# Kernel tuning notes

Measured on AMD Instinct MI355X. Metric: run time of the kernel, lower is better.

The kernel has to match this reference:

```python
import jax, jax.numpy as jnp
import numpy as np
from jax import lax

EPS = 1e-5

def bn(x, g, b):
    # training-mode BatchNorm2d over (N, H, W)
    m = jnp.mean(x, axis=(0, 2, 3), keepdims=True)
    v = jnp.var(x, axis=(0, 2, 3), keepdims=True)
    return (x - m) * lax.rsqrt(v + EPS) * g[None, :, None, None] + b[None, :, None, None]

def conv1x1(x, W):
    # x: [b,c,h,w], W: [o,c]
    return jnp.einsum('bchw,oc->bohw', x, W)

def conv3x3(x, W):
    # W: [o,i,3,3]
    return lax.conv_general_dilated(x, W, (1, 1), 'SAME',
                                    dimension_numbers=('NCHW', 'OIHW', 'NCHW'))

def lga(x, Wqkv, Wproj, g, b):
    # LinearGlobalAttention: O(N) global attention
    bsz, c, h, w = x.shape
    qkv = conv1x1(x, Wqkv)                       # [b, 3c, h, w]
    q, k, v = jnp.split(qkv, 3, axis=1)
    q = q.reshape(bsz, c, h * w)                 # [b, c, N]
    k = jax.nn.softmax(k.reshape(bsz, c, h * w), axis=-1)
    v = v.reshape(bsz, c, h * w)
    ctx = jnp.einsum('bcn,bdn->bcd', k, v)       # [b, c, c]
    out = jnp.einsum('bcd,bcn->bdn', ctx, q)     # context^T @ q -> [b, c, N]
    out = out.reshape(bsz, c, h, w)
    return jax.nn.relu(bn(conv1x1(out, Wproj), g, b))


def setup_inputs() -> dict:
    key = jax.random.key(0)
    ks = jax.random.split(key, 12)
    B, Cin, Cout, H, W = 16, 128, 256, 64, 64
    wd = Cout // 4  # branch width = 64
    sc = 0.05
    inp = {
        'x': jax.random.normal(ks[0], (B, Cin, H, W), jnp.float32),
        'W_sc': jax.random.normal(ks[1], (Cout, Cin), jnp.float32) * sc,
        'g_sc': jnp.ones((Cout,), jnp.float32),
        'b_sc': jnp.zeros((Cout,), jnp.float32),
        'W1': jax.random.normal(ks[2], (Cout, Cin), jnp.float32) * sc,
        'g1': jnp.ones((Cout,), jnp.float32),
        'b1': jnp.zeros((Cout,), jnp.float32),
        'Wb0': jax.random.normal(ks[3], (wd, wd), jnp.float32) * sc,
        'gb0': jnp.ones((wd,), jnp.float32),
        'bb0': jnp.zeros((wd,), jnp.float32),
        'Wb1': jax.random.normal(ks[4], (wd, wd, 3, 3), jnp.float32) * sc,
        'gb1': jnp.ones((wd,), jnp.float32),
        'bb1': jnp.zeros((wd,), jnp.float32),
        'Wqkv2': jax.random.normal(ks[5], (3 * wd, wd), jnp.float32) * sc,
        'Wproj2': jax.random.normal(ks[6], (wd, wd), jnp.float32) * sc,
        'ga2': jnp.ones((wd,), jnp.float32),
        'ba2': jnp.zeros((wd,), jnp.float32),
        'Wqkv3': jax.random.normal(ks[7], (3 * wd, wd), jnp.float32) * sc,
        'Wproj3': jax.random.normal(ks[8], (wd, wd), jnp.float32) * sc,
        'ga3': jnp.ones((wd,), jnp.float32),
        'ba3': jnp.zeros((wd,), jnp.float32),
        'W2': jax.random.normal(ks[9], (Cout, Cout), jnp.float32) * sc,
        'g2': jnp.ones((Cout,), jnp.float32),
        'b2': jnp.zeros((Cout,), jnp.float32),
    }
    return inp


def reference(x, W_sc, g_sc, b_sc, W1, g1, b1,
              Wb0, gb0, bb0, Wb1, gb1, bb1,
              Wqkv2, Wproj2, ga2, ba2,
              Wqkv3, Wproj3, ga3, ba3,
              W2, g2, b2):
    residual = bn(conv1x1(x, W_sc), g_sc, b_sc)
    h = jax.nn.relu(bn(conv1x1(x, W1), g1, b1))      # [b, 256, H, W]
    s0, s1, s2, s3 = jnp.split(h, 4, axis=1)          # width = 64 each
    o0 = jax.nn.relu(bn(conv1x1(s0, Wb0), gb0, bb0))  # k=1 branch
    o1 = jax.nn.relu(bn(conv3x3(s1, Wb1), gb1, bb1))  # k=3 branch
    o2 = lga(s2, Wqkv2, Wproj2, ga2, ba2)             # k=5 -> attention
    o3 = lga(s3, Wqkv3, Wproj3, ga3, ba3)             # k=7 -> attention
    out = jnp.concatenate([o0, o1, o2, o3], axis=1)
    out = bn(conv1x1(out, W2), g2, b2) + residual
    return jax.nn.relu(out)
```

## Files before the change

kernel.cpp:

```cpp
#include <hip/hip_runtime.h>
#include <hip/hip_bf16.h>

using bf16 = __hip_bfloat16;
typedef __bf16 bf16v8 __attribute__((ext_vector_type(8)));
typedef float f32x4 __attribute__((ext_vector_type(4)));

#define HW 4096
#define ROWS 65536
#define BRSTRIDE 4194304

#define AS1 const __attribute__((address_space(1))) void*
#define AS3 __attribute__((address_space(3))) void*

__global__ void r4_cvt_w(const float* __restrict__ Wsc, const float* __restrict__ W1,
                         const float* __restrict__ Wb0,
                         const float* __restrict__ Wqkv2, const float* __restrict__ Wqkv3,
                         const float* __restrict__ W2, const float* __restrict__ Wb1,
                         bf16* __restrict__ wbase, bf16* __restrict__ wp,
                         float* __restrict__ stats) {
    int i = blockIdx.x * 256 + threadIdx.x;
    if (i < 2048) stats[i] = 0.f;
    if (i < 159744) {
        const float* s; int off;
        if      (i < 32768)  { s = Wsc;   off = i; }
        else if (i < 65536)  { s = W1;    off = i - 32768; }
        else if (i < 69632)  { s = Wb0;   off = i - 65536; }
        else if (i < 81920)  { s = Wqkv2; off = i - 69632; }
        else if (i < 94208)  { s = Wqkv3; off = i - 81920; }
        else                 { s = W2;    off = i - 94208; }
        wbase[i] = __float2bfloat16(s[off]);
    } else {
        int k = i - 159744;
        int tap = k / 4096, rem = k % 4096;
        int o = rem >> 6, c = rem & 63;
        wp[k] = __float2bfloat16(Wb1[(size_t)(o * 64 + c) * 9 + tap]);
    }
}

__global__ void r4_cvt_x(const float* __restrict__ x, bf16* __restrict__ xT) {
    __shared__ bf16 tile[64 * 65];
    int b = blockIdx.z, c0 = blockIdx.y * 64, n0 = blockIdx.x * 64;
    int t = threadIdx.x;
#pragma unroll
    for (int i = 0; i < 4; i++) {
        int idx = i * 256 + t;
        int cc = idx >> 4, n4 = (idx & 15) * 4;
        float4 v = *(const float4*)&x[((size_t)(b * 128 + c0 + cc)) * HW + n0 + n4];
        tile[(n4 + 0) * 65 + cc] = __float2bfloat16(v.x);
        tile[(n4 + 1) * 65 + cc] = __float2bfloat16(v.y);
        tile[(n4 + 2) * 65 + cc] = __float2bfloat16(v.z);
        tile[(n4 + 3) * 65 + cc] = __float2bfloat16(v.w);
    }
    __syncthreads();
#pragma unroll
    for (int i = 0; i < 2; i++) {
        int u = i * 256 + t;
        int nn = u >> 3, p = u & 7;
        bf16v8 v;
#pragma unroll
        for (int j = 0; j < 8; j++) v[j] = (__bf16)tile[nn * 65 + p * 8 + j];
        *(bf16v8*)&xT[((size_t)(b * HW + n0 + nn)) * 128 + c0 + p * 8] = v;
    }
}

template <int KK>
__global__ __launch_bounds__(256) void ga_gemm(
        const bf16* __restrict__ A, int a_stride,
        const bf16* __restrict__ W, int w_stride,
        bf16* __restrict__ out0, bf16* __restrict__ out1, int split,
        int out_stride,
        float* __restrict__ stat0, float* __restrict__ stat1,
        int scol0, int scol1,
        const float* __restrict__ tsums,
        const float* __restrict__ tg0, const float* __restrict__ tb0,
        const float* __restrict__ tg1, const float* __restrict__ tb1,
        const float* __restrict__ tg2, const float* __restrict__ tb2,
        const float* __restrict__ tg3, const float* __restrict__ tb3) {
    __shared__ bf16 shmem[128 * 136];
    __shared__ float sredS[256], sredQ[256];
    __shared__ float scS[256], shS[256];
    bf16* As = shmem;
    bf16* Ws = shmem + 8192;

    int t = threadIdx.x;
    int wave = t >> 6, lane = t & 63;
    int lo = lane & 15, quad = lane >> 4;
    int wr = wave >> 1, wc = wave & 1;
    int b = blockIdx.z;
    long grow = (long)b * HW + blockIdx.x * 128;
    int o0 = blockIdx.y * 128;
    const bf16* Wb = W + (long)o0 * w_stride;

    if (tsums) {
        int qi = t >> 6, ci = t & 63;
        const float* gp = qi == 0 ? tg0 : qi == 1 ? tg1 : qi == 2 ? tg2 : tg3;
        const float* bp = qi == 0 ? tb0 : qi == 1 ? tb1 : qi == 2 ? tb2 : tb3;
        float mean = tsums[t] * (1.f / 65536.f);
        float var  = tsums[256 + t] * (1.f / 65536.f) - mean * mean;
        float s = gp[ci] * rsqrtf(var + 1e-5f);
        scS[t] = s; shS[t] = bp[ci] - mean * s;
    }

    f32x4 acc[4][4];
#pragma unroll
    for (int m = 0; m < 4; m++)
#pragma unroll
        for (int n = 0; n < 4; n++) acc[m][n] = (f32x4){0.f, 0.f, 0.f, 0.f};

#pragma unroll
    for (int ph = 0; ph < KK / 64; ph++) {
        int k0 = ph * 64;
#pragma unroll
        for (int j = 0; j < 4; j++) {
            int i = j * 4 + wave;
            int ci = i * 64 + lane;
            int R = ci >> 3, cc = ci & 7;
            int sw = ((cc ^ (R & 7)) << 3);
            __builtin_amdgcn_global_load_lds(
                (AS1)(A + (grow + R) * (long)a_stride + k0 + sw),
                (AS3)(As + i * 512), 16, 0, 0);
            __builtin_amdgcn_global_load_lds(
                (AS1)(Wb + (long)R * w_stride + k0 + sw),
                (AS3)(Ws + i * 512), 16, 0, 0);
        }
        asm volatile("s_waitcnt vmcnt(0)" ::: "memory");
        __syncthreads();
        if (tsums) {
#pragma unroll
            for (int i = 0; i < 4; i++) {
                int ci = i * 256 + t;
                int R = ci >> 3, p = ci & 7;
                int chb = k0 + ((p ^ (R & 7)) << 3);
                bf16v8 v = *(const bf16v8*)&As[R * 64 + p * 8];
#pragma unroll
                for (int j = 0; j < 8; j++) {
                    float f = (float)v[j] * scS[chb + j] + shS[chb + j];
                    v[j] = (__bf16)fmaxf(f, 0.f);
                }
                *(bf16v8*)&As[R * 64 + p * 8] = v;
            }
            __syncthreads();
        }
#pragma unroll
        for (int ks = 0; ks < 64; ks += 32) {
            int kk = (ks >> 3) + quad;
            bf16v8 av[4], wv[4];
#pragma unroll
            for (int m = 0; m < 4; m++) {
                int R = wr * 64 + m * 16 + lo;
                av[m] = *(const bf16v8*)&As[R * 64 + ((kk ^ (R & 7)) << 3)];
            }
#pragma unroll
            for (int n = 0; n < 4; n++) {
                int R = wc * 64 + n * 16 + lo;
                wv[n] = *(const bf16v8*)&Ws[R * 64 + ((kk ^ (R & 7)) << 3)];
            }
#pragma unroll
            for (int m = 0; m < 4; m++)
#pragma unroll
                for (int n = 0; n < 4; n++)
                    acc[m][n] = __builtin_amdgcn_mfma_f32_16x16x32_bf16(av[m], wv[n], acc[m][n], 0, 0, 0);
        }
        __syncthreads();
    }

    bf16* Ot = shmem;
#pragma unroll
    for (int m = 0; m < 4; m++)
#pragma unroll
        for (int n = 0; n < 4; n++)
#pragma unroll
            for (int r = 0; r < 4; r++)
                Ot[(wr * 64 + m * 16 + quad * 4 + r) * 136 + wc * 64 + n * 16 + lo] =
                    __float2bfloat16(acc[m][n][r]);
    __syncthreads();
    bool low = o0 < split;
    bf16* op = low ? out0 : out1;
    int oc0 = low ? o0 : o0 - split;
#pragma unroll
    for (int i = 0; i < 8; i++) {
        int u = i * 256 + t;
        int lr = u >> 4, cg = u & 15;
        *(bf16v8*)&op[(grow + lr) * (long)out_stride + oc0 + cg * 8] =
            *(const bf16v8*)&Ot[lr * 136 + cg * 8];
    }
    if (stat0) {
        int c = t & 127, half = t >> 7;
        float s = 0.f, q = 0.f;
#pragma unroll
        for (int r = 0; r < 64; r++) {
            float v = __bfloat162float(Ot[(half * 64 + r) * 136 + c]);
            s += v; q += v * v;
        }
        sredS[t] = s; sredQ[t] = q;
        __syncthreads();
        if (t < 128) {
            float ss = sredS[t] + sredS[t + 128];
            float qq = sredQ[t] + sredQ[t + 128];
            float* st = low ? stat0 : stat1;
            int ci = (low ? scol0 + o0 : scol1 + o0 - split) + c;
            atomicAdd(&st[ci], ss);
            atomicAdd(&st[256 + ci], qq);
        }
    }
}

__global__ __launch_bounds__(256) void gq_gemm(
        const bf16* __restrict__ y1,
        const bf16* __restrict__ wq2, const bf16* __restrict__ wq3,
        const bf16* __restrict__ wb0,
        bf16* __restrict__ qs, bf16* __restrict__ ks, bf16* __restrict__ vs,
        bf16* __restrict__ obuf, float* __restrict__ stats,
        const float* __restrict__ asums,
        const float* __restrict__ g1, const float* __restrict__ b1) {
    __shared__ bf16 shmem[128 * 64 + 64 * 64];
    __shared__ float scS[64], shS[64];
    bf16* As = shmem;
    bf16* Ws = shmem + 8192;
    float* sredS = (float*)(shmem + 9216);
    float* sredQ = sredS + 256;

    int t = threadIdx.x;
    int wave = t >> 6, lane = t & 63;
    int lo = lane & 15, quad = lane >> 4;
    int b = blockIdx.z, y = blockIdx.y;
    long grow = (long)b * HW + blockIdx.x * 128;

    const bf16* Ab; const bf16* Wb; bf16* outp; int ostride; float* st; int col0;
    if (y == 6) {
        Ab = y1; Wb = wb0; outp = obuf; ostride = 256; st = stats; col0 = 0;
    } else {
        int br = y / 3, sel = y - br * 3;
        col0 = 128 + br * 64;
        Ab = y1 + col0;
        Wb = (br ? wq3 : wq2) + sel * 4096;
        outp = (sel == 0 ? qs : sel == 1 ? ks : vs) + (long)br * BRSTRIDE;
        ostride = 64; st = nullptr;
    }
    if (t < 64) {
        int ch = col0 + t;
        float mean = asums[ch] * (1.f / 65536.f);
        float var  = asums[256 + ch] * (1.f / 65536.f) - mean * mean;
        float s = g1[ch] * rsqrtf(var + 1e-5f);
        scS[t] = s; shS[t] = b1[ch] - mean * s;
    }

    f32x4 acc[2][4];
#pragma unroll
    for (int m = 0; m < 2; m++)
#pragma unroll
        for (int n = 0; n < 4; n++) acc[m][n] = (f32x4){0.f, 0.f, 0.f, 0.f};

#pragma unroll
    for (int j = 0; j < 4; j++) {
        int i = j * 4 + wave;
        int ci = i * 64 + lane;
        int R = ci >> 3, cc = ci & 7;
        __builtin_amdgcn_global_load_lds(
            (AS1)(Ab + (grow + R) * 256L + ((cc ^ (R & 7)) << 3)),
            (AS3)(As + i * 512), 16, 0, 0);
    }
#pragma unroll
    for (int j = 0; j < 2; j++) {
        int ci = (j * 4 + wave) * 64 + lane;
        int R = ci >> 3, cc = ci & 7;
        __builtin_amdgcn_global_load_lds(
            (AS1)(Wb + R * 64 + ((cc ^ (R & 7)) << 3)),
            (AS3)(Ws + (j * 4 + wave) * 512), 16, 0, 0);
    }
    asm volatile("s_waitcnt vmcnt(0)" ::: "memory");
    __syncthreads();
#pragma unroll
    for (int i = 0; i < 4; i++) {
        int ci = i * 256 + t;
        int R = ci >> 3, p = ci & 7;
        int chb = (p ^ (R & 7)) << 3;
        bf16v8 v = *(const bf16v8*)&As[R * 64 + p * 8];
#pragma unroll
        for (int j = 0; j < 8; j++) {
            float f = (float)v[j] * scS[chb + j] + shS[chb + j];
            v[j] = (__bf16)fmaxf(f, 0.f);
        }
        *(bf16v8*)&As[R * 64 + p * 8] = v;
    }
    __syncthreads();

#pragma unroll
    for (int ks_ = 0; ks_ < 64; ks_ += 32) {
        int kk = (ks_ >> 3) + quad;
        bf16v8 av[2], wv[4];
#pragma unroll
        for (int m = 0; m < 2; m++) {
            int R = wave * 32 + m * 16 + lo;
            av[m] = *(const bf16v8*)&As[R * 64 + ((kk ^ (R & 7)) << 3)];
        }
#pragma unroll
        for (int n = 0; n < 4; n++) {
            int o = n * 16 + lo;
            wv[n] = *(const bf16v8*)&Ws[o * 64 + ((kk ^ (o & 7)) << 3)];
        }
#pragma unroll
        for (int m = 0; m < 2; m++)
#pragma unroll
            for (int n = 0; n < 4; n++)
                acc[m][n] = __builtin_amdgcn_mfma_f32_16x16x32_bf16(av[m], wv[n], acc[m][n], 0, 0, 0);
    }
    __syncthreads();

    bf16* Ot = shmem;
#pragma unroll
    for (int m = 0; m < 2; m++)
#pragma unroll
        for (int n = 0; n < 4; n++)
#pragma unroll
            for (int r = 0; r < 4; r++)
                Ot[(wave * 32 + m * 16 + quad * 4 + r) * 72 + n * 16 + lo] =
                    __float2bfloat16(acc[m][n][r]);
    __syncthreads();
#pragma unroll
    for (int i = 0; i < 4; i++) {
        int u = i * 256 + t;
        int lr = u >> 3, cg = u & 7;
        *(bf16v8*)&outp[(grow + lr) * (long)ostride + cg * 8] =
            *(const bf16v8*)&Ot[lr * 72 + cg * 8];
    }
    if (st) {
        int c = t & 63, qtr = t >> 6;
        float s = 0.f, q = 0.f;
#pragma unroll
        for (int r = 0; r < 32; r++) {
            float v = __bfloat162float(Ot[(qtr * 32 + r) * 72 + c]);
            s += v; q += v * v;
        }
        sredS[t] = s; sredQ[t] = q;
        __syncthreads();
        if (t < 64) {
            float ss = sredS[t] + sredS[t + 64] + sredS[t + 128] + sredS[t + 192];
            float qq = sredQ[t] + sredQ[t + 64] + sredQ[t + 128] + sredQ[t + 192];
            atomicAdd(&st[t], ss);
            atomicAdd(&st[256 + t], qq);
        }
    }
}

__global__ __launch_bounds__(256) void gp_gemm(
        const bf16* __restrict__ qs, const bf16* __restrict__ M,
        bf16* __restrict__ obuf, float* __restrict__ stats) {
    __shared__ bf16 shmem[128 * 64 + 64 * 64];
    bf16* As = shmem;
    bf16* Ws = shmem + 8192;
    float* sredS = (float*)(shmem + 9216);
    float* sredQ = sredS + 256;

    int t = threadIdx.x;
    int wave = t >> 6, lane = t & 63;
    int lo = lane & 15, quad = lane >> 4;
    int b = blockIdx.z, y = blockIdx.y;
    long grow = (long)b * HW + blockIdx.x * 128;
    const bf16* Ab = qs + (long)y * BRSTRIDE;
    const bf16* Wb = M + y * 65536 + (long)b * 4096;
    int oc0 = 128 + y * 64;

    f32x4 acc[2][4];
#pragma unroll
    for (int m = 0; m < 2; m++)
#pragma unroll
        for (int n = 0; n < 4; n++) acc[m][n] = (f32x4){0.f, 0.f, 0.f, 0.f};

#pragma unroll
    for (int j = 0; j < 4; j++) {
        int i = j * 4 + wave;
        int ci = i * 64 + lane;
        int R = ci >> 3, cc = ci & 7;
        __builtin_amdgcn_global_load_lds(
            (AS1)(Ab + (grow + R) * 64L + ((cc ^ (R & 7)) << 3)),
            (AS3)(As + i * 512), 16, 0, 0);
    }
#pragma unroll
    for (int j = 0; j < 2; j++) {
        int ci = (j * 4 + wave) * 64 + lane;
        int R = ci >> 3, cc = ci & 7;
        __builtin_amdgcn_global_load_lds(
            (AS1)(Wb + R * 64 + ((cc ^ (R & 7)) << 3)),
            (AS3)(Ws + (j * 4 + wave) * 512), 16, 0, 0);
    }
    asm volatile("s_waitcnt vmcnt(0)" ::: "memory");
    __syncthreads();

#pragma unroll
    for (int ks_ = 0; ks_ < 64; ks_ += 32) {
        int kk = (ks_ >> 3) + quad;
        bf16v8 av[2], wv[4];
#pragma unroll
        for (int m = 0; m < 2; m++) {
            int R = wave * 32 + m * 16 + lo;
            av[m] = *(const bf16v8*)&As[R * 64 + ((kk ^ (R & 7)) << 3)];
        }
#pragma unroll
        for (int n = 0; n < 4; n++) {
            int o = n * 16 + lo;
            wv[n] = *(const bf16v8*)&Ws[o * 64 + ((kk ^ (o & 7)) << 3)];
        }
#pragma unroll
        for (int m = 0; m < 2; m++)
#pragma unroll
            for (int n = 0; n < 4; n++)
                acc[m][n] = __builtin_amdgcn_mfma_f32_16x16x32_bf16(av[m], wv[n], acc[m][n], 0, 0, 0);
    }
    __syncthreads();

    bf16* Ot = shmem;
#pragma unroll
    for (int m = 0; m < 2; m++)
#pragma unroll
        for (int n = 0; n < 4; n++)
#pragma unroll
            for (int r = 0; r < 4; r++)
                Ot[(wave * 32 + m * 16 + quad * 4 + r) * 72 + n * 16 + lo] =
                    __float2bfloat16(acc[m][n][r]);
    __syncthreads();
#pragma unroll
    for (int i = 0; i < 4; i++) {
        int u = i * 256 + t;
        int lr = u >> 3, cg = u & 7;
        *(bf16v8*)&obuf[(grow + lr) * 256L + oc0 + cg * 8] =
            *(const bf16v8*)&Ot[lr * 72 + cg * 8];
    }
    {
        int c = t & 63, qtr = t >> 6;
        float s = 0.f, q = 0.f;
#pragma unroll
        for (int r = 0; r < 32; r++) {
            float v = __bfloat162float(Ot[(qtr * 32 + r) * 72 + c]);
            s += v; q += v * v;
        }
        sredS[t] = s; sredQ[t] = q;
        __syncthreads();
        if (t < 64) {
            float ss = sredS[t] + sredS[t + 64] + sredS[t + 128] + sredS[t + 192];
            float qq = sredQ[t] + sredQ[t + 64] + sredQ[t + 128] + sredQ[t + 192];
            atomicAdd(&stats[oc0 + t], ss);
            atomicAdd(&stats[256 + oc0 + t], qq);
        }
    }
}

__global__ __launch_bounds__(256) void r12_conv3(
        const bf16* __restrict__ hT, const bf16* __restrict__ wp,
        bf16* __restrict__ obuf, float* __restrict__ stat,
        const float* __restrict__ asums,
        const float* __restrict__ g1, const float* __restrict__ b1) {
    __shared__ bf16 As[6 * 66 * 64];
    __shared__ bf16 Wt[9 * 64 * 64];
    __shared__ float sredS[256], sredQ[256];
    __shared__ float scS[64], shS[64];

    int t = threadIdx.x;
    int wave = t >> 6, lane = t & 63;
    int lo = lane & 15, quad = lane >> 4;
    int b = blockIdx.y, y0 = blockIdx.x * 4;

    if (t < 64) {
        int ch = 64 + t;
        float mean = asums[ch] * (1.f / 65536.f);
        float var  = asums[256 + ch] * (1.f / 65536.f) - mean * mean;
        float s = g1[ch] * rsqrtf(var + 1e-5f);
        scS[t] = s; shS[t] = b1[ch] - mean * s;
    }

#pragma unroll
    for (int j = 0; j < 18; j++) {
        int i = j * 4 + wave;
        int ci = i * 64 + lane;
        int tap = ci >> 9, rem = ci & 511, o = rem >> 3, ck = rem & 7;
        __builtin_amdgcn_global_load_lds(
            (AS1)(wp + tap * 4096 + o * 64 + ((ck ^ (o & 7)) << 3)),
            (AS3)(Wt + i * 512), 16, 0, 0);
    }
#pragma unroll
    for (int j = 0; j < 12; j++) {
        int i = j * 4 + wave;
        int row = i >> 3, seg = i & 7;
        int yy = y0 - 1 + row;
        if (yy >= 0 && yy < 64) {
            int xg = seg * 8 + (lane >> 3), ck = lane & 7;
            __builtin_amdgcn_global_load_lds(
                (AS1)(hT + ((long)b * HW + yy * 64 + xg) * 256 + 64 + ((ck ^ (xg & 7)) << 3)),
                (AS3)(As + row * 4224 + 64 + seg * 512), 16, 0, 0);
        } else {
            *(bf16v8*)&As[row * 4224 + 64 + seg * 512 + lane * 8] = (bf16v8){0,0,0,0,0,0,0,0};
        }
    }
    if (t < 96) {
        int yr = t >> 4, side = (t >> 3) & 1, ck = t & 7;
        *(bf16v8*)&As[yr * 4224 + (side ? 65 : 0) * 64 + ck * 8] = (bf16v8){0,0,0,0,0,0,0,0};
    }
    asm volatile("s_waitcnt vmcnt(0)" ::: "memory");
    __syncthreads();
#pragma unroll
    for (int i = 0; i < 12; i++) {
        int ci = i * 256 + t;
        int row = ci >> 9, rem = ci & 511;
        int xg = rem >> 3, p = rem & 7;
        int yy = y0 - 1 + row;
        if (yy >= 0 && yy < 64) {
            int chb = (p ^ (xg & 7)) << 3;
            bf16v8 v = *(const bf16v8*)&As[row * 4224 + (xg + 1) * 64 + p * 8];
#pragma unroll
            for (int j = 0; j < 8; j++) {
                float f = (float)v[j] * scS[chb + j] + shS[chb + j];
                v[j] = (__bf16)fmaxf(f, 0.f);
            }
            *(bf16v8*)&As[row * 4224 + (xg + 1) * 64 + p * 8] = v;
        }
    }
    __syncthreads();

    f32x4 acc[4][4];
#pragma unroll
    for (int m = 0; m < 4; m++)
#pragma unroll
        for (int n = 0; n < 4; n++) acc[m][n] = (f32x4){0.f, 0.f, 0.f, 0.f};

#pragma unroll
    for (int tap = 0; tap < 9; tap++) {
        int dy = tap / 3 - 1, dx = tap % 3 - 1;
        int yr = wave + 1 + dy;
#pragma unroll
        for (int ks8 = 0; ks8 < 8; ks8 += 4) {
            int kk = ks8 + quad;
            bf16v8 wv[4];
#pragma unroll
            for (int ot = 0; ot < 4; ot++) {
                int o = ot * 16 + lo;
                wv[ot] = *(const bf16v8*)&Wt[tap * 4096 + o * 64 + ((kk ^ (o & 7)) << 3)];
            }
#pragma unroll
            for (int m = 0; m < 4; m++) {
                int xp = m * 16 + lo + dx;
                bf16v8 av = *(const bf16v8*)&As[yr * 4224 + (xp + 1) * 64 + ((kk ^ (xp & 7)) << 3)];
#pragma unroll
                for (int ot = 0; ot < 4; ot++)
                    acc[m][ot] = __builtin_amdgcn_mfma_f32_16x16x32_bf16(av, wv[ot], acc[m][ot], 0, 0, 0);
            }
        }
    }
    __syncthreads();

    bf16* Ot = As;
#pragma unroll
    for (int m = 0; m < 4; m++)
#pragma unroll
        for (int ot = 0; ot < 4; ot++)
#pragma unroll
            for (int r = 0; r < 4; r++)
                Ot[(wave * 64 + m * 16 + quad * 4 + r) * 72 + ot * 16 + lo] =
                    __float2bfloat16(acc[m][ot][r]);
    __syncthreads();

    long grow = (long)b * HW + y0 * 64;
#pragma unroll
    for (int i = 0; i < 8; i++) {
        int u = i * 256 + t;
        int lr = u >> 3, cg = u & 7;
        *(bf16v8*)&obuf[(grow + lr) * 256 + 64 + cg * 8] = *(const bf16v8*)&Ot[lr * 72 + cg * 8];
    }
    {
        int c = t & 63, qtr = t >> 6;
        float s = 0.f, q = 0.f;
#pragma unroll
        for (int r = 0; r < 64; r++) {
            float v = __bfloat162float(Ot[(qtr * 64 + r) * 72 + c]);
            s += v; q += v * v;
        }
        sredS[t] = s; sredQ[t] = q;
        __syncthreads();
        if (t < 64) {
            float ss = sredS[t] + sredS[t + 64] + sredS[t + 128] + sredS[t + 192];
            float qq = sredQ[t] + sredQ[t + 64] + sredQ[t + 128] + sredQ[t + 192];
            atomicAdd(&stat[64 + t], ss);
            atomicAdd(&stat[256 + 64 + t], qq);
        }
    }
}

__global__ __launch_bounds__(256) void r14_softctx(
        const bf16* __restrict__ ks_t, const bf16* __restrict__ vs_t,
        float* __restrict__ ctx_p, float* __restrict__ lpart) {
    __shared__ bf16 Ks[64 * 136];
    __shared__ bf16 Vs[64 * 136];
    float* red = (float*)Ks;
    int t = threadIdx.x;
    int wave = t >> 6, lane = t & 63;
    int lo = lane & 15, quad = lane >> 4;
    int b = blockIdx.y, bx = blockIdx.x, z = blockIdx.z;
    const bf16* kb = ks_t + (long)z * BRSTRIDE;
    const bf16* vb = vs_t + (long)z * BRSTRIDE;

    f32x4 acc[4];
#pragma unroll
    for (int ot = 0; ot < 4; ot++) acc[ot] = (f32x4){0.f, 0.f, 0.f, 0.f};
    float sm[8];
#pragma unroll
    for (int j = 0; j < 8; j++) sm[j] = 0.f;

    for (int it = 0; it < 2; it++) {
        long n0 = ((long)bx * 2 + it) * 128;
        __syncthreads();
#pragma unroll
        for (int sub = 0; sub < 4; sub++) {
            int r = sub * 32 + (t >> 3), cg = t & 7;
            long row = (long)b * HW + n0 + r;
            bf16v8 k8 = *(const bf16v8*)(kb + row * 64 + cg * 8);
            bf16v8 v8 = *(const bf16v8*)(vb + row * 64 + cg * 8);
#pragma unroll
            for (int j = 0; j < 8; j++) {
                int c = cg * 8 + j;
                float e = expf((float)k8[j]);
                sm[j] += e;
                Ks[c * 136 + r] = __float2bfloat16(e);
                Vs[c * 136 + r] = (bf16)v8[j];
            }
        }
        __syncthreads();
#pragma unroll
        for (int ks = 0; ks < 128; ks += 32) {
            bf16v8 av = *(const bf16v8*)&Ks[(wave * 16 + lo) * 136 + ks + quad * 8];
#pragma unroll
            for (int ot = 0; ot < 4; ot++) {
                bf16v8 bv = *(const bf16v8*)&Vs[(ot * 16 + lo) * 136 + ks + quad * 8];
                acc[ot] = __builtin_amdgcn_mfma_f32_16x16x32_bf16(av, bv, acc[ot], 0, 0, 0);
            }
        }
    }
    long blk = ((long)z * 16 + b) * 16 + bx;
#pragma unroll
    for (int ot = 0; ot < 4; ot++) {
#pragma unroll
        for (int r = 0; r < 4; r++) {
            int c = wave * 16 + quad * 4 + r;
            int d = ot * 16 + lo;
            ctx_p[(blk * 64 + c) * 64 + d] = acc[ot][r];
        }
    }
    {
        __syncthreads();
        int rg = t >> 3, cg = t & 7;
#pragma unroll
        for (int j = 0; j < 8; j++) red[rg * 64 + cg * 8 + j] = sm[j];
        __syncthreads();
        if (t < 64) {
            float s = 0.f;
#pragma unroll
            for (int i = 0; i < 32; i++) s += red[i * 64 + t];
            lpart[blk * 64 + t] = s;
        }
    }
}

__global__ __launch_bounds__(256) void r15_mproj(
        const float* __restrict__ Wp2, const float* __restrict__ Wp3,
        const float* __restrict__ ctx_p, const float* __restrict__ lpart,
        bf16* __restrict__ M) {
    __shared__ float ctxS[16 * 68];
    __shared__ float ilS[16];
    int b = blockIdx.x, qq = blockIdx.y, z = blockIdx.z, t = threadIdx.x;
    int e = t & 63, cg = t >> 6;
    const float* Wp = z ? Wp3 : Wp2;
    long zb = (long)z * 16 + b;
#pragma unroll
    for (int i = 0; i < 4; i++) {
        int u = i * 256 + t;
        int c_l = u >> 6, d = u & 63;
        float s = 0.f;
#pragma unroll
        for (int p = 0; p < 16; p++)
            s += ctx_p[((zb * 16 + p) * 64 + qq * 16 + c_l) * 64 + d];
        ctxS[c_l * 68 + d] = s;
    }
    if (t < 16) {
        float l = 0.f;
#pragma unroll
        for (int p = 0; p < 16; p++)
            l += lpart[(zb * 16 + p) * 64 + qq * 16 + t];
        ilS[t] = 1.f / l;
    }
    float wreg[64];
#pragma unroll
    for (int i = 0; i < 16; i++) {
        float4 v = *(const float4*)&Wp[e * 64 + i * 4];
        wreg[i * 4 + 0] = v.x; wreg[i * 4 + 1] = v.y;
        wreg[i * 4 + 2] = v.z; wreg[i * 4 + 3] = v.w;
    }
    __syncthreads();
#pragma unroll
    for (int ci = 0; ci < 4; ci++) {
        int c_l = cg * 4 + ci;
        float a = 0.f;
#pragma unroll
        for (int dg = 0; dg < 16; dg++) {
            float4 cv = *(const float4*)&ctxS[c_l * 68 + dg * 4];
            a += wreg[dg * 4 + 0] * cv.x + wreg[dg * 4 + 1] * cv.y
               + wreg[dg * 4 + 2] * cv.z + wreg[dg * 4 + 3] * cv.w;
        }
        M[(long)z * 65536 + (long)b * 4096 + e * 64 + qq * 16 + c_l] =
            __float2bfloat16(a * ilS[c_l]);
    }
}

__global__ void r6_final(const bf16* __restrict__ y2, const bf16* __restrict__ ysc,
                         const float* __restrict__ s2sums, const float* __restrict__ scsums,
                         const float* __restrict__ g2, const float* __restrict__ b2,
                         const float* __restrict__ gsc, const float* __restrict__ bsc,
                         float* __restrict__ out) {
    __shared__ float lo_[64 * 65];
    __shared__ float sc2[64], sh2[64], scc[64], shc[64];
    int b = blockIdx.z, c0 = blockIdx.y * 64, n0 = blockIdx.x * 64;
    int t = threadIdx.x;
    if (t < 64) {
        int ch = c0 + t;
        float m2 = s2sums[ch] * (1.f / 65536.f);
        float v2 = s2sums[256 + ch] * (1.f / 65536.f) - m2 * m2;
        float s = g2[ch] * rsqrtf(v2 + 1e-5f);
        sc2[t] = s; sh2[t] = b2[ch] - m2 * s;
        float mc = scsums[ch] * (1.f / 65536.f);
        float vc = scsums[256 + ch] * (1.f / 65536.f) - mc * mc;
        float s2_ = gsc[ch] * rsqrtf(vc + 1e-5f);
        scc[t] = s2_; shc[t] = bsc[ch] - mc * s2_;
    }
    __syncthreads();
    for (int half = 0; half < 2; half++) {
        int r = half * 32 + (t >> 3), cc = (t & 7) * 8;
        long row = (long)b * HW + n0 + r;
        bf16v8 a8 = *(const bf16v8*)&y2[row * 256 + c0 + cc];
        bf16v8 s8 = *(const bf16v8*)&ysc[row * 256 + c0 + cc];
#pragma unroll
        for (int j = 0; j < 8; j++) {
            int c = cc + j;
            float v = (float)a8[j] * sc2[c] + sh2[c] + (float)s8[j] * scc[c] + shc[c];
            lo_[c * 65 + r] = fmaxf(v, 0.f);
        }
    }
    __syncthreads();
#pragma unroll
    for (int i = 0; i < 4; i++) {
        int idx = i * 256 + t;
        int c = idx >> 4, r4 = (idx & 15) * 4;
        float4 w;
        w.x = lo_[c * 65 + r4 + 0];
        w.y = lo_[c * 65 + r4 + 1];
        w.z = lo_[c * 65 + r4 + 2];
        w.w = lo_[c * 65 + r4 + 3];
        *(float4*)&out[((long)(b * 256 + c0 + c)) * HW + n0 + r4] = w;
    }
}

extern "C" void kernel_launch(void* const* d_in, const int* in_sizes, int n_in,
                              void* d_out, int out_size, void* d_ws, size_t ws_size,
                              hipStream_t stream) {
    const float* x     = (const float*)d_in[0];
    const float* Wsc   = (const float*)d_in[1];
    const float* gsc   = (const float*)d_in[2];
    const float* bsc   = (const float*)d_in[3];
    const float* W1    = (const float*)d_in[4];
    const float* g1    = (const float*)d_in[5];
    const float* b1    = (const float*)d_in[6];
    const float* Wb0   = (const float*)d_in[7];
    const float* gb0   = (const float*)d_in[8];
    const float* bb0   = (const float*)d_in[9];
    const float* Wb1   = (const float*)d_in[10];
    const float* gb1   = (const float*)d_in[11];
    const float* bb1   = (const float*)d_in[12];
    const float* Wqkv2 = (const float*)d_in[13];
    const float* Wproj2= (const float*)d_in[14];
    const float* ga2   = (const float*)d_in[15];
    const float* ba2   = (const float*)d_in[16];
    const float* Wqkv3 = (const float*)d_in[17];
    const float* Wproj3= (const float*)d_in[18];
    const float* ga3   = (const float*)d_in[19];
    const float* ba3   = (const float*)d_in[20];
    const float* W2    = (const float*)d_in[21];
    const float* g2    = (const float*)d_in[22];
    const float* b2    = (const float*)d_in[23];

    char* ws = (char*)d_ws;
    float* stats = (float*)ws;
    bf16*  M     = (bf16*)(ws + 32768);
    bf16*  wbase = (bf16*)(ws + 294912);
    bf16*  wsc_b = wbase;
    bf16*  wb0_b = wbase + 65536;
    bf16*  wq2_b = wbase + 69632;
    bf16*  wq3_b = wbase + 81920;
    bf16*  w2_b  = wbase + 94208;
    bf16*  wb1p  = (bf16*)(ws + 614400);
    bf16*  xT    = (bf16*)(ws + 1048576);
    bf16*  vs    = (bf16*)(ws + 1048576);
    bf16*  ysc   = (bf16*)(ws + 17825792);
    bf16*  y1    = (bf16*)(ws + 51380224);
    float* ctx_p = (float*)(ws + 51380224);
    float* lpart = (float*)(ws + 51380224 + 8388608);
    bf16*  y2    = y1;
    bf16*  obuf  = (bf16*)d_out;
    bf16*  qs    = (bf16*)((char*)d_out + 33554432);
    bf16*  ks    = (bf16*)((char*)d_out + 50331648);

    r4_cvt_w<<<dim3(768), 256, 0, stream>>>(Wsc, W1, Wb0, Wqkv2, Wqkv3, W2, Wb1,
                                            wbase, wb1p, stats);
    r4_cvt_x<<<dim3(64, 2, 16), 256, 0, stream>>>(x, xT);

    ga_gemm<128><<<dim3(32, 4, 16), 256, 0, stream>>>(
        xT, 128, wsc_b, 128,
        ysc, y1, 256, 256, stats, stats + 512, 0, 0,
        nullptr, nullptr, nullptr, nullptr, nullptr, nullptr, nullptr, nullptr, nullptr);

    r12_conv3<<<dim3(16, 16), 256, 0, stream>>>(y1, wb1p, obuf, stats + 1024,
                                                stats + 512, g1, b1);
    gq_gemm<<<dim3(32, 7, 16), 256, 0, stream>>>(
        y1, wq2_b, wq3_b, wb0_b, qs, ks, vs, obuf, stats + 1024,
        stats + 512, g1, b1);

    r14_softctx<<<dim3(16, 16, 2), 256, 0, stream>>>(ks, vs, ctx_p, lpart);
    r15_mproj<<<dim3(16, 4, 2), 256, 0, stream>>>(Wproj2, Wproj3, ctx_p, lpart, M);
    gp_gemm<<<dim3(32, 2, 16), 256, 0, stream>>>(qs, M, obuf, stats + 1024);

    ga_gemm<256><<<dim3(32, 2, 16), 256, 0, stream>>>(
        obuf, 256, w2_b, 256,
        y2, y2, 1 << 28, 256, stats + 1536, stats + 1536, 0, 0,
        stats + 1024, gb0, bb0, gb1, bb1, ga2, ba2, ga3, ba3);

    r6_final<<<dim3(64, 4, 16), 256, 0, stream>>>(y2, ysc, stats + 1536, stats + 0,
                                                  g2, b2, gsc, bsc, (float*)d_out);
}
```

Baseline: 283.8 us.

## Fuse K/V projection with softmax-exp and context GEMM, dropping K/V buffers

Adds a gkv_ctx kernel that computes the K and V projections for each 128-row tile and applies exp to K in registers. It stages both transposed in LDS and immediately accumulates the partial context matrix and softmax denominators, so K and V are never written to or re-read from global memory. gq_gemm now only produces Q and the k=1 branch output, and the separate r14_softctx launch is removed. The cost is that r15_mproj must reduce twice as many context partials, and the new kernel needs more LDS per block, which may lower occupancy.

```diff
diff --git a/kernel.cpp b/kernel.cpp
--- a/kernel.cpp
+++ b/kernel.cpp
@@ -209,7 +209,7 @@
         const bf16* __restrict__ y1,
         const bf16* __restrict__ wq2, const bf16* __restrict__ wq3,
         const bf16* __restrict__ wb0,
-        bf16* __restrict__ qs, bf16* __restrict__ ks, bf16* __restrict__ vs,
+        bf16* __restrict__ qs,
         bf16* __restrict__ obuf, float* __restrict__ stats,
         const float* __restrict__ asums,
         const float* __restrict__ g1, const float* __restrict__ b1) {
@@ -227,14 +227,13 @@
     long grow = (long)b * HW + blockIdx.x * 128;
 
     const bf16* Ab; const bf16* Wb; bf16* outp; int ostride; float* st; int col0;
-    if (y == 6) {
+    if (y == 2) {
         Ab = y1; Wb = wb0; outp = obuf; ostride = 256; st = stats; col0 = 0;
     } else {
-        int br = y / 3, sel = y - br * 3;
-        col0 = 128 + br * 64;
+        col0 = 128 + y * 64;
         Ab = y1 + col0;
-        Wb = (br ? wq3 : wq2) + sel * 4096;
-        outp = (sel == 0 ? qs : sel == 1 ? ks : vs) + (long)br * BRSTRIDE;
+        Wb = (y ? wq3 : wq2);
+        outp = qs + (long)y * BRSTRIDE;
         ostride = 64; st = nullptr;
     }
     if (t < 64) {
@@ -340,6 +339,163 @@
             atomicAdd(&st[t], ss);
             atomicAdd(&st[256 + t], qq);
         }
+    }
+}
+
+__global__ __launch_bounds__(256) void gkv_ctx(
+        const bf16* __restrict__ y1,
+        const bf16* __restrict__ wq2, const bf16* __restrict__ wq3,
+        float* __restrict__ ctx_p, float* __restrict__ lpart,
+        const float* __restrict__ asums,
+        const float* __restrict__ g1, const float* __restrict__ b1) {
+    __shared__ bf16 As[128 * 64];
+    __shared__ bf16 Ws[2 * 64 * 64];
+    __shared__ bf16 Kt[64 * 136];
+    __shared__ bf16 Vt[64 * 136];
+    __shared__ float scS[64], shS[64];
+    float* red = (float*)As;
+
+    int t = threadIdx.x;
+    int wave = t >> 6, lane = t & 63;
+    int lo = lane & 15, quad = lane >> 4;
+    int b = blockIdx.z, br = blockIdx.y, bx = blockIdx.x;
+    long grow = (long)b * HW + bx * 128;
+    int col0 = 128 + br * 64;
+    const bf16* Ab = y1 + col0;
+    const bf16* Wk = (br ? wq3 : wq2) + 4096;
+    const bf16* Wv = (br ? wq3 : wq2) + 8192;
+
+    if (t < 64) {
+        int ch = col0 + t;
+        float mean = asums[ch] * (1.f / 65536.f);
+        float var  = asums[256 + ch] * (1.f / 65536.f) - mean * mean;
+        float s = g1[ch] * rsqrtf(var + 1e-5f);
+        scS[t] = s; shS[t] = b1[ch] - mean * s;
+    }
+
+#pragma unroll
+    for (int j = 0; j < 4; j++) {
+        int i = j * 4 + wave;
+        int ci = i * 64 + lane;
+        int R = ci >> 3, cc = ci & 7;
+        __builtin_amdgcn_global_load_lds(
+            (AS1)(Ab + (grow + R) * 256L + ((cc ^ (R & 7)) << 3)),
+            (AS3)(As + i * 512), 16, 0, 0);
+    }
+#pragma unroll
+    for (int j = 0; j < 2; j++) {
+        int ci = (j * 4 + wave) * 64 + lane;
+        int R = ci >> 3, cc = ci & 7;
+        __builtin_amdgcn_global_load_lds(
+            (AS1)(Wk + R * 64 + ((cc ^ (R & 7)) << 3)),
+            (AS3)(Ws + (j * 4 + wave) * 512), 16, 0, 0);
+    }
+#pragma unroll
+    for (int j = 0; j < 2; j++) {
+        int ci = (j * 4 + wave) * 64 + lane;
+        int R = ci >> 3, cc = ci & 7;
+        __builtin_amdgcn_global_load_lds(
+            (AS1)(Wv + R * 64 + ((cc ^ (R & 7)) << 3)),
+            (AS3)(Ws + 4096 + (j * 4 + wave) * 512), 16, 0, 0);
+    }
+    asm volatile("s_waitcnt vmcnt(0)" ::: "memory");
+    __syncthreads();
+#pragma unroll
+    for (int i = 0; i < 4; i++) {
+        int ci = i * 256 + t;
+        int R = ci >> 3, p = ci & 7;
+        int chb = (p ^ (R & 7)) << 3;
+        bf16v8 v = *(const bf16v8*)&As[R * 64 + p * 8];
+#pragma unroll
+        for (int j = 0; j < 8; j++) {
+            float f = (float)v[j] * scS[chb + j] + shS[chb + j];
+            v[j] = (__bf16)fmaxf(f, 0.f);
+        }
+        *(bf16v8*)&As[R * 64 + p * 8] = v;
+    }
+    __syncthreads();
+
+    f32x4 aK[2][4], aV[2][4];
+#pragma unroll
+    for (int m = 0; m < 2; m++)
+#pragma unroll
+        for (int n = 0; n < 4; n++) {
+            aK[m][n] = (f32x4){0.f, 0.f, 0.f, 0.f};
+            aV[m][n] = (f32x4){0.f, 0.f, 0.f, 0.f};
+        }
+#pragma unroll
+    for (int ks_ = 0; ks_ < 64; ks_ += 32) {
+        int kk = (ks_ >> 3) + quad;
+        bf16v8 av[2], wk[4], wv[4];
+#pragma unroll
+        for (int m = 0; m < 2; m++) {
+            int R = wave * 32 + m * 16 + lo;
+            av[m] = *(const bf16v8*)&As[R * 64 + ((kk ^ (R & 7)) << 3)];
+        }
+#pragma unroll
+        for (int n = 0; n < 4; n++) {
+            int o = n * 16 + lo;
+            wk[n] = *(const bf16v8*)&Ws[o * 64 + ((kk ^ (o & 7)) << 3)];
+            wv[n] = *(const bf16v8*)&Ws[4096 + o * 64 + ((kk ^ (o & 7)) << 3)];
+        }
+#pragma unroll
+        for (int m = 0; m < 2; m++)
+#pragma unroll
+            for (int n = 0; n < 4; n++) {
+                aK[m][n] = __builtin_amdgcn_mfma_f32_16x16x32_bf16(av[m], wk[n], aK[m][n], 0, 0, 0);
+                aV[m][n] = __builtin_amdgcn_mfma_f32_16x16x32_bf16(av[m], wv[n], aV[m][n], 0, 0, 0);
+            }
+    }
+    __syncthreads();
+
+    float sm[4] = {0.f, 0.f, 0.f, 0.f};
+#pragma unroll
+    for (int m = 0; m < 2; m++)
+#pragma unroll
+        for (int n = 0; n < 4; n++)
+#pragma unroll
+            for (int r = 0; r < 4; r++) {
+                int row = wave * 32 + m * 16 + quad * 4 + r;
+                int col = n * 16 + lo;
+                float e = expf(aK[m][n][r]);
+                sm[n] += e;
+                Kt[col * 136 + row] = __float2bfloat16(e);
+                Vt[col * 136 + row] = __float2bfloat16(aV[m][n][r]);
+            }
+    {
+        int g = wave * 4 + quad;
+#pragma unroll
+        for (int n = 0; n < 4; n++) red[g * 64 + n * 16 + lo] = sm[n];
+    }
+    __syncthreads();
+
+    f32x4 acc[4];
+#pragma unroll
+    for (int ot = 0; ot < 4; ot++) acc[ot] = (f32x4){0.f, 0.f, 0.f, 0.f};
+#pragma unroll
+    for (int ks_ = 0; ks_ < 128; ks_ += 32) {
+        bf16v8 av = *(const bf16v8*)&Kt[(wave * 16 + lo) * 136 + ks_ + quad * 8];
+#pragma unroll
+        for (int ot = 0; ot < 4; ot++) {
+            bf16v8 bv = *(const bf16v8*)&Vt[(ot * 16 + lo) * 136 + ks_ + quad * 8];
+            acc[ot] = __builtin_amdgcn_mfma_f32_16x16x32_bf16(av, bv, acc[ot], 0, 0, 0);
+        }
+    }
+    long blk = ((long)br * 16 + b) * 32 + bx;
+#pragma unroll
+    for (int ot = 0; ot < 4; ot++) {
+#pragma unroll
+        for (int r = 0; r < 4; r++) {
+            int c = wave * 16 + quad * 4 + r;
+            int d = ot * 16 + lo;
+            ctx_p[(blk * 64 + c) * 64 + d] = acc[ot][r];
+        }
+    }
+    if (t < 64) {
+        float l = 0.f;
+#pragma unroll
+        for (int g = 0; g < 16; g++) l += red[g * 64 + t];
+        lpart[blk * 64 + t] = l;
     }
 }
 
@@ -584,80 +740,6 @@
     }
 }
 
-__global__ __launch_bounds__(256) void r14_softctx(
-        const bf16* __restrict__ ks_t, const bf16* __restrict__ vs_t,
-        float* __restrict__ ctx_p, float* __restrict__ lpart) {
-    __shared__ bf16 Ks[64 * 136];
-    __shared__ bf16 Vs[64 * 136];
-    float* red = (float*)Ks;
-    int t = threadIdx.x;
-    int wave = t >> 6, lane = t & 63;
-    int lo = lane & 15, quad = lane >> 4;
-    int b = blockIdx.y, bx = blockIdx.x, z = blockIdx.z;
-    const bf16* kb = ks_t + (long)z * BRSTRIDE;
-    const bf16* vb = vs_t + (long)z * BRSTRIDE;
-
-    f32x4 acc[4];
-#pragma unroll
-    for (int ot = 0; ot < 4; ot++) acc[ot] = (f32x4){0.f, 0.f, 0.f, 0.f};
-    float sm[8];
-#pragma unroll
-    for (int j = 0; j < 8; j++) sm[j] = 0.f;
-
-    for (int it = 0; it < 2; it++) {
-        long n0 = ((long)bx * 2 + it) * 128;
-        __syncthreads();
-#pragma unroll
-        for (int sub = 0; sub < 4; sub++) {
-            int r = sub * 32 + (t >> 3), cg = t & 7;
-            long row = (long)b * HW + n0 + r;
-            bf16v8 k8 = *(const bf16v8*)(kb + row * 64 + cg * 8);
-            bf16v8 v8 = *(const bf16v8*)(vb + row * 64 + cg * 8);
-#pragma unroll
-            for (int j = 0; j < 8; j++) {
-                int c = cg * 8 + j;
-                float e = expf((float)k8[j]);
-                sm[j] += e;
-                Ks[c * 136 + r] = __float2bfloat16(e);
-                Vs[c * 136 + r] = (bf16)v8[j];
-            }
-        }
-        __syncthreads();
-#pragma unroll
-        for (int ks = 0; ks < 128; ks += 32) {
-            bf16v8 av = *(const bf16v8*)&Ks[(wave * 16 + lo) * 136 + ks + quad * 8];
-#pragma unroll
-            for (int ot = 0; ot < 4; ot++) {
-                bf16v8 bv = *(const bf16v8*)&Vs[(ot * 16 + lo) * 136 + ks + quad * 8];
-                acc[ot] = __builtin_amdgcn_mfma_f32_16x16x32_bf16(av, bv, acc[ot], 0, 0, 0);
-            }
-        }
-    }
-    long blk = ((long)z * 16 + b) * 16 + bx;
-#pragma unroll
-    for (int ot = 0; ot < 4; ot++) {
-#pragma unroll
-        for (int r = 0; r < 4; r++) {
-            int c = wave * 16 + quad * 4 + r;
-            int d = ot * 16 + lo;
-            ctx_p[(blk * 64 + c) * 64 + d] = acc[ot][r];
-        }
-    }
-    {
-        __syncthreads();
-        int rg = t >> 3, cg = t & 7;
-#pragma unroll
-        for (int j = 0; j < 8; j++) red[rg * 64 + cg * 8 + j] = sm[j];
-        __syncthreads();
-        if (t < 64) {
-            float s = 0.f;
-#pragma unroll
-            for (int i = 0; i < 32; i++) s += red[i * 64 + t];
-            lpart[blk * 64 + t] = s;
-        }
-    }
-}
-
 __global__ __launch_bounds__(256) void r15_mproj(
         const float* __restrict__ Wp2, const float* __restrict__ Wp3,
         const float* __restrict__ ctx_p, const float* __restrict__ lpart,
@@ -674,15 +756,15 @@
         int c_l = u >> 6, d = u & 63;
         float s = 0.f;
 #pragma unroll
-        for (int p = 0; p < 16; p++)
-            s += ctx_p[((zb * 16 + p) * 64 + qq * 16 + c_l) * 64 + d];
+        for (int p = 0; p < 32; p++)
+            s += ctx_p[((zb * 32 + p) * 64 + qq * 16 + c_l) * 64 + d];
         ctxS[c_l * 68 + d] = s;
     }
     if (t < 16) {
         float l = 0.f;
 #pragma unroll
-        for (int p = 0; p < 16; p++)
-            l += lpart[(zb * 16 + p) * 64 + qq * 16 + t];
+        for (int p = 0; p < 32; p++)
+            l += lpart[(zb * 32 + p) * 64 + qq * 16 + t];
         ilS[t] = 1.f / l;
     }
     float wreg[64];
@@ -793,16 +875,14 @@
     bf16*  wq3_b = wbase + 81920;
     bf16*  w2_b  = wbase + 94208;
     bf16*  wb1p  = (bf16*)(ws + 614400);
+    float* lpart = (float*)(ws + 688128);
     bf16*  xT    = (bf16*)(ws + 1048576);
-    bf16*  vs    = (bf16*)(ws + 1048576);
+    float* ctx_p = (float*)(ws + 1048576);
     bf16*  ysc   = (bf16*)(ws + 17825792);
     bf16*  y1    = (bf16*)(ws + 51380224);
-    float* ctx_p = (float*)(ws + 51380224);
-    float* lpart = (float*)(ws + 51380224 + 8388608);
     bf16*  y2    = y1;
     bf16*  obuf  = (bf16*)d_out;
     bf16*  qs    = (bf16*)((char*)d_out + 33554432);
-    bf16*  ks    = (bf16*)((char*)d_out + 50331648);
 
     r4_cvt_w<<<dim3(768), 256, 0, stream>>>(Wsc, W1, Wb0, Wqkv2, Wqkv3, W2, Wb1,
                                             wbase, wb1p, stats);
@@ -815,11 +895,12 @@
 
     r12_conv3<<<dim3(16, 16), 256, 0, stream>>>(y1, wb1p, obuf, stats + 1024,
                                                 stats + 512, g1, b1);
-    gq_gemm<<<dim3(32, 7, 16), 256, 0, stream>>>(
-        y1, wq2_b, wq3_b, wb0_b, qs, ks, vs, obuf, stats + 1024,
+    gkv_ctx<<<dim3(32, 2, 16), 256, 0, stream>>>(
+        y1, wq2_b, wq3_b, ctx_p, lpart, stats + 512, g1, b1);
+    gq_gemm<<<dim3(32, 3, 16), 256, 0, stream>>>(
+        y1, wq2_b, wq3_b, wb0_b, qs, obuf, stats + 1024,
         stats + 512, g1, b1);
 
-    r14_softctx<<<dim3(16, 16, 2), 256, 0, stream>>>(ks, vs, ctx_p, lpart);
     r15_mproj<<<dim3(16, 4, 2), 256, 0, stream>>>(Wproj2, Wproj3, ctx_p, lpart, M);
     gp_gemm<<<dim3(32, 2, 16), 256, 0, stream>>>(qs, M, obuf, stats + 1024);
 
```

Measured after the change: 291.1 us. 1.03x slower.
